# Kernel optimization log

Hardware: AMD Instinct MI355X
Metric: run time of the kernel (lower is better)

## Reference

```python
import jax, jax.numpy as jnp
import numpy as np

BS, TLEN, NNODE, DIM = 32, 6, 4, 1500
HID = 128; D2 = 2 * HID
LSTMH, LSTMO, KCONV = 64, 128, 3
CONV_OUT = 191
DECAY = 0.7
WIN, STRIDES = (2, 2), (1, 2)
FEAT_IN = LSTMO * CONV_OUT  # 24448


def _bn(x, p, axis):
    # eval-mode BatchNorm: p = [gamma, beta, running_mean, running_var] stacked [4, C]
    sh = [1] * x.ndim; sh[axis] = -1
    g, b, m, v = (p[i].reshape(sh) for i in range(4))
    return (x - m) * (g * jax.lax.rsqrt(v + 1e-5)) + b


def _conv1d(x, w, pad):  # x [B,C,L], w [O,I,K]
    return jax.lax.conv_general_dilated(x, w, (1,), [(pad, pad)],
                                        dimension_numbers=('NCH', 'OIH', 'NCH'))


def _maxpool2(x):  # MaxPool1d(kernel=2, stride=2, padding=1) with -inf padding
    x = jnp.pad(x, ((0, 0), (0, 0), (1, 1)), constant_values=-jnp.inf)
    return jax.lax.reduce_window(x, -jnp.inf, jax.lax.max, (1, 1, 2), (1, 1, 2), 'VALID')


def _mpnn_block(x, w, s, gw, gb, bnA, tw, tb, bnM):
    # x: [bs, tlen, ns, d]; Conv_GraphST windowing + dot-graph + masked adj + 1-hop MPNN + mean pool
    bs, tlen, ns, d = x.shape
    nw = (tlen - w) // s + 1
    con = jnp.stack([x[:, j * s:j * s + w] for j in range(nw)], axis=1)  # [bs,nw,w,ns,d]
    Xc = con.reshape(bs * nw, w * ns, d)  # node index = t*ns + sensor (time-major)
    f = Xc @ gw + gb
    N = w * ns
    eye = jnp.eye(N, dtype=x.dtype)
    Adj = jnp.einsum('bnd,bmd->bnm', f, f)
    Adj = jax.nn.softmax(jax.nn.leaky_relu(Adj - eye * 1e8), axis=-1) + eye
    t = jnp.arange(N) // ns
    mask = DECAY ** jnp.abs(t[:, None] - t[None, :]).astype(x.dtype)  # Mask_Matrix decay
    Adj = Adj * mask
    Xb = _bn(Xc, bnA, -1)  # BN over feature channel (transpose-BN-transpose in torch)
    h = jnp.einsum('bnm,bmd->bnd', Adj, Xb) @ tw + tb
    h = jax.nn.leaky_relu(_bn(h, bnM, -1))
    return h.reshape(bs, nw, w, ns, -1).mean(axis=2)  # mean pool over window-time


def _pos_encoding(tlen, d):
    pos = jnp.arange(tlen, dtype=jnp.float32)[:, None]
    div = jnp.exp(jnp.arange(0, d, 2, dtype=jnp.float32) * (-np.log(100.0) / d))
    pe = jnp.zeros((tlen, d), jnp.float32)
    return pe.at[:, 0::2].set(jnp.sin(pos * div)).at[:, 1::2].set(jnp.cos(pos * div))


def reference(X, conv1_w, bn1, conv2_w, bn2, conv3_w, bn3,
              map2_w, map2_b, bn_map2,
              g1_w, g1_b, bnA1, th1_w, th1_b, bnM1,
              g2_w, g2_b, bnA2, th2_w, th2_b, bnM2,
              fc1_w, fc1_b, fc2_w, fc2_b, fc3_w, fc3_b, fc4_w, fc4_b):
    X = X.reshape(BS, TLEN, NNODE, -1)
    B = BS * TLEN * NNODE
    a = jnp.transpose(X.reshape(B, -1, 1), (0, 2, 1))  # [B,1,L]
    a = _maxpool2(jax.nn.relu(_bn(_conv1d(a, conv1_w, KCONV // 2), bn1, 1)))
    a = _maxpool2(jax.nn.relu(_bn(_conv1d(a, conv2_w, 2), bn2, 1)))
    a = _maxpool2(jax.nn.relu(_bn(_conv1d(a, conv3_w, 3), bn3, 1)))  # [B,LSTMO,CONV_OUT]
    a = a.reshape(B, -1)
    a = _bn(a @ map2_w + map2_b, bn_map2, -1)
    a = a.reshape(BS, TLEN, NNODE, D2)
    a = a + _pos_encoding(TLEN, D2)[None, :, None, :]  # PE over time, per (batch, node)
    out1 = _mpnn_block(a, WIN[0], STRIDES[0], g1_w, g1_b, bnA1, th1_w, th1_b, bnM1)  # [32,5,4,128]
    out2 = _mpnn_block(a, WIN[1], STRIDES[1], g2_w, g2_b, bnA2, th2_w, th2_b, bnM2)  # [32,3,4,128]
    feats = jnp.concatenate([out1.reshape(BS, -1), out2.reshape(BS, -1)], axis=-1)  # [32,4096]
    h = jax.nn.relu(feats @ fc1_w + fc1_b)
    h = jax.nn.relu(h @ fc2_w + fc2_b)
    h = jax.nn.relu(h @ fc3_w + fc3_b)
    return h @ fc4_w + fc4_b


def setup_inputs():
    key = jax.random.key(0)
    ks = iter(jax.random.split(key, 80))
    def rn(shape, scale=1.0):
        return scale * jax.random.normal(next(ks), shape, jnp.float32)
    def bn(c):
        return jnp.stack([1.0 + 0.1 * rn((c,)), 0.1 * rn((c,)), 0.1 * rn((c,)),
                          1.0 + 0.5 * jax.random.uniform(next(ks), (c,), jnp.float32)])
    def lin(i, o):
        return rn((i, o), 1.0 / np.sqrt(i))
    return {
        'X': rn((BS, TLEN, NNODE, DIM)),
        'conv1_w': rn((LSTMH, 1, KCONV), 0.3),
        'bn1': bn(LSTMH),
        'conv2_w': rn((2 * LSTMH, LSTMH, KCONV), 1.0 / np.sqrt(LSTMH * KCONV)),
        'bn2': bn(2 * LSTMH),
        'conv3_w': rn((LSTMO, 2 * LSTMH, KCONV), 1.0 / np.sqrt(2 * LSTMH * KCONV)),
        'bn3': bn(LSTMO),
        'map2_w': lin(FEAT_IN, D2), 'map2_b': rn((D2,), 0.01), 'bn_map2': bn(D2),
        'g1_w': lin(D2, D2), 'g1_b': rn((D2,), 0.01), 'bnA1': bn(D2),
        'th1_w': lin(D2, HID), 'th1_b': rn((HID,), 0.01), 'bnM1': bn(HID),
        'g2_w': lin(D2, D2), 'g2_b': rn((D2,), 0.01), 'bnA2': bn(D2),
        'th2_w': lin(D2, HID), 'th2_b': rn((HID,), 0.01), 'bnM2': bn(HID),
        'fc1_w': lin(4096, D2), 'fc1_b': rn((D2,), 0.01),
        'fc2_w': lin(D2, D2), 'fc2_b': rn((D2,), 0.01),
        'fc3_w': lin(D2, HID), 'fc3_b': rn((HID,), 0.01),
        'fc4_w': lin(HID, 5), 'fc4_b': rn((5,), 0.01),
    }
```

## Files before the change

### kernel.cpp

```cpp
#include <hip/hip_runtime.h>
#include <hip/hip_bf16.h>

#define L1X   1500
#define L1P   751
#define C1    64
#define L2P   377
#define C2    128
#define L3P   191
#define C3    128
#define FEATK 24448
#define D2    256
#define HIDN  128

#define SK      32
#define KCHUNK  764
#define NIT     191

typedef __attribute__((ext_vector_type(8))) short bf16x8;
typedef __attribute__((ext_vector_type(4))) float f32x4;

__device__ __forceinline__ short f2bf(float x) {
    union { float f; unsigned u; } v; v.f = x;
    unsigned r = (v.u + 0x7FFFu + ((v.u >> 16) & 1u)) >> 16;
    return (short)r;
}
__device__ __forceinline__ float bf2f(short s) {
    union { float f; unsigned u; } v; v.u = ((unsigned)(unsigned short)s) << 16;
    return v.f;
}

template<int IC, int KB>
__global__ __launch_bounds__(256)
void k_wprep(const float* __restrict__ w, short* __restrict__ WtHi,
             short* __restrict__ WtLo)
{
    int idx = blockIdx.x * 256 + threadIdx.x;
    if (idx >= 3 * KB * 4 * 128 * 8) return;
    int i    = idx & 7;
    int rest = idx >> 3;
    int c    = rest & 127; rest >>= 7;
    int sub  = rest & 3;   rest >>= 2;
    int kb   = rest % KB;
    int tap  = rest / KB;
    int ic   = kb * 32 + sub * 8 + i;
    float x  = w[(c * IC + ic) * 3 + tap];
    short h  = f2bf(x);
    WtHi[idx] = h;
    WtLo[idx] = f2bf(x - bf2f(h));
}

template<int IC, int KB, int CONVLEN, int POOLLEN>
__device__ __forceinline__
void conv_mfma_core(const short* __restrict__ WtHi, const short* __restrict__ WtLo,
                    const short* lhi, const short* llo,
                    const float* sc, const float* bc,
                    float* __restrict__ outp, int P0)
{
    const int lane = threadIdx.x & 63;
    const int wave = threadIdx.x >> 6;
    const int l15  = lane & 15;
    const int sub  = lane >> 4;

    f32x4 acc[2][8];
    #pragma unroll
    for (int mf = 0; mf < 2; ++mf)
        #pragma unroll
        for (int nf = 0; nf < 8; ++nf)
            acc[mf][nf] = (f32x4){0.f, 0.f, 0.f, 0.f};

    #pragma unroll
    for (int tap = 0; tap < 3; ++tap) {
        #pragma unroll
        for (int kb = 0; kb < KB; ++kb) {
            bf16x8 ah[2], al[2];
            #pragma unroll
            for (int mf = 0; mf < 2; ++mf) {
                int r = wave * 32 + mf * 16 + l15 + tap;
                int chunk = (kb * 4 + sub) ^ (r & 7);
                int off = r * IC + chunk * 8;
                ah[mf] = *(const bf16x8*)(lhi + off);
                al[mf] = *(const bf16x8*)(llo + off);
            }
            const short* wbh = WtHi + (size_t)(((tap * KB + kb) * 4 + sub) * 128) * 8;
            const short* wbl = WtLo + (size_t)(((tap * KB + kb) * 4 + sub) * 128) * 8;
            #pragma unroll
            for (int nf = 0; nf < 8; ++nf) {
                bf16x8 bh = *(const bf16x8*)(wbh + (nf * 16 + l15) * 8);
                bf16x8 bl = *(const bf16x8*)(wbl + (nf * 16 + l15) * 8);
                #pragma unroll
                for (int mf = 0; mf < 2; ++mf) {
                    acc[mf][nf] = __builtin_amdgcn_mfma_f32_16x16x32_bf16(ah[mf], bh, acc[mf][nf], 0, 0, 0);
                    acc[mf][nf] = __builtin_amdgcn_mfma_f32_16x16x32_bf16(ah[mf], bl, acc[mf][nf], 0, 0, 0);
                    acc[mf][nf] = __builtin_amdgcn_mfma_f32_16x16x32_bf16(al[mf], bh, acc[mf][nf], 0, 0, 0);
                }
            }
        }
    }

    #pragma unroll
    for (int mf = 0; mf < 2; ++mf) {
        int mbase = wave * 32 + mf * 16 + sub * 4;
        #pragma unroll
        for (int nf = 0; nf < 8; ++nf) {
            int c = nf * 16 + l15;
            float s = sc[c], bb = bc[c];
            float v[4];
            #pragma unroll
            for (int rg = 0; rg < 4; ++rg) {
                int p = P0 + mbase + rg;
                float x = fmaxf(acc[mf][nf][rg] * s + bb, 0.f);
                v[rg] = (p >= 0 && p < CONVLEN) ? x : 0.f;
            }
            int i0 = (P0 + mbase + 1) >> 1;
            float u0 = fmaxf(v[0], v[1]);
            float u1 = fmaxf(v[2], v[3]);
            if (i0 < POOLLEN)     outp[(size_t)i0 * 128 + c] = u0;
            if (i0 + 1 < POOLLEN) outp[(size_t)(i0 + 1) * 128 + c] = u1;
        }
    }
}

__global__ __launch_bounds__(256)
void k_conv2_mfma(const float* __restrict__ X, const float* __restrict__ w1,
                  const float* __restrict__ bn1,
                  const short* __restrict__ Wt2hi, const short* __restrict__ Wt2lo,
                  const float* __restrict__ bn2, float* __restrict__ pool2t,
                  int b_off)
{
    const int blk = blockIdx.x;
    const int bl  = blk / 6, t = blk % 6;
    const int b   = b_off + bl;
    const int P0  = 128 * t - 1;
    const int T0  = 128 * t - 3;
    const int X0  = 256 * t - 8;

    __shared__ __align__(16) float xw[264];
    __shared__ __align__(16) short t1h[130 * 64];
    __shared__ __align__(16) short t1l[130 * 64];
    __shared__ float sb1s[64], sb1b[64], sc2[128], bc2[128];

    const int tid = threadIdx.x;
    for (int g = tid; g < 262; g += 256) {
        int xi = X0 + g;
        xw[g] = (xi >= 0 && xi < L1X) ? X[(size_t)b * L1X + xi] : 0.f;
    }
    if (tid < 64) {
        float s = bn1[tid] * rsqrtf(bn1[192 + tid] + 1e-5f);
        sb1s[tid] = s;
        sb1b[tid] = bn1[64 + tid] - bn1[128 + tid] * s;
    }
    if (tid < 128) {
        float s = bn2[tid] * rsqrtf(bn2[384 + tid] + 1e-5f);
        sc2[tid] = s;
        bc2[tid] = bn2[128 + tid] - bn2[256 + tid] * s;
    }
    __syncthreads();

    for (int idx = tid; idx < 130 * 64; idx += 256) {
        int r = idx >> 6, c = idx & 63;
        int tt = T0 + r;
        float val = 0.f;
        if (tt >= 0 && tt <= 750) {
            float wk0 = w1[c * 3], wk1 = w1[c * 3 + 1], wk2 = w1[c * 3 + 2];
            float s = sb1s[c], bias = sb1b[c];
            float v0 = 0.f, v1 = 0.f;
            int li = 2 * r;
            if (tt >= 1)
                v0 = fmaxf((wk0 * xw[li] + wk1 * xw[li + 1] + wk2 * xw[li + 2]) * s + bias, 0.f);
            if (tt <= 749)
                v1 = fmaxf((wk0 * xw[li + 1] + wk1 * xw[li + 2] + wk2 * xw[li + 3]) * s + bias, 0.f);
            val = fmaxf(v0, v1);
        }
        short h = f2bf(val);
        int chunk = (c >> 3) ^ (r & 7);
        int off = r * 64 + chunk * 8 + (c & 7);
        t1h[off] = h;
        t1l[off] = f2bf(val - bf2f(h));
    }
    __syncthreads();

    conv_mfma_core<64, 2, 753, 377>(Wt2hi, Wt2lo, t1h, t1l, sc2, bc2,
                                    pool2t + (size_t)bl * L2P * 128, P0);
}

__global__ __launch_bounds__(256)
void k_conv3_mfma(const float* __restrict__ pool2t,
                  const short* __restrict__ Wt3hi, const short* __restrict__ Wt3lo,
                  const float* __restrict__ bn3, float* __restrict__ pool3t,
                  int b_off)
{
    const int blk = blockIdx.x;
    const int bl  = blk / 3, t = blk % 3;
    const int b   = b_off + bl;
    const int P0  = 128 * t - 1;
    const int I0  = 128 * t - 4;

    __shared__ __align__(16) short t2h[130 * 128];
    __shared__ __align__(16) short t2l[130 * 128];
    __shared__ float sc3[128], bc3[128];

    const int tid = threadIdx.x;
    if (tid < 128) {
        float s = bn3[tid] * rsqrtf(bn3[384 + tid] + 1e-5f);
        sc3[tid] = s;
        bc3[tid] = bn3[128 + tid] - bn3[256 + tid] * s;
    }

    const float* src = pool2t + (size_t)bl * L2P * 128;
    for (int idx = tid; idx < 130 * 32; idx += 256) {
        int r = idx >> 5, q = idx & 31;
        int pr = I0 + r;
        float4 v = make_float4(0.f, 0.f, 0.f, 0.f);
        if (pr >= 0 && pr < L2P) v = *(const float4*)(src + (size_t)pr * 128 + q * 4);
        int chunk = (q >> 1) ^ (r & 7);
        int off = r * 128 + chunk * 8 + (q & 1) * 4;
        *(short4*)(t2h + off) = make_short4(f2bf(v.x), f2bf(v.y), f2bf(v.z), f2bf(v.w));
        short l0 = f2bf(v.x - bf2f(f2bf(v.x)));
        short l1 = f2bf(v.y - bf2f(f2bf(v.y)));
        short l2 = f2bf(v.z - bf2f(f2bf(v.z)));
        short l3 = f2bf(v.w - bf2f(f2bf(v.w)));
        *(short4*)(t2l + off) = make_short4(l0, l1, l2, l3);
    }
    __syncthreads();

    conv_mfma_core<128, 4, 381, 191>(Wt3hi, Wt3lo, t2h, t2l, sc3, bc3,
                                     pool3t + (size_t)b * L3P * 128, P0);
}

__global__ __launch_bounds__(256)
void k_map2_gemm(const float* __restrict__ A, const float* __restrict__ W,
                 float* __restrict__ part)
{
    const int bid = blockIdx.x;
    const int kt  = bid / 24;
    const int rem = bid % 24;
    const int mt  = rem >> 1;
    const int nt  = rem & 1;

    __shared__ __align__(16) float At[2][4][68];
    __shared__ __align__(16) float Bt[2][4][128];

    const int tid = threadIdx.x;
    const int m0  = (tid & 15) * 4;
    const int n0  = (tid >> 4) * 8;

    const int arow = tid >> 2;
    const int akk  = tid & 3;
    const int bk   = tid >> 6;
    const int bc   = (tid & 63) * 2;

    const float* Aptr = A + (size_t)(mt * 64 + arow) * FEATK + kt * KCHUNK + akk;

    #define BROW(it) (W + (size_t)((((kt*KCHUNK + (it)*4 + bk) & 127) * 191 + \
                                    ((kt*KCHUNK + (it)*4 + bk) >> 7))) * D2 + nt*128 + bc)

    float acc[4][8];
    #pragma unroll
    for (int i = 0; i < 4; ++i)
        #pragma unroll
        for (int j = 0; j < 8; ++j) acc[i][j] = 0.f;

    float  a_reg = Aptr[0];
    float2 b_reg = *(const float2*)(BROW(0));
    At[0][akk][arow] = a_reg;
    *(float2*)&Bt[0][bk][bc] = b_reg;

    int cur = 0;
    for (int it = 0; it < NIT; ++it) {
        __syncthreads();
        if (it + 1 < NIT) {
            a_reg = Aptr[(it + 1) * 4];
            b_reg = *(const float2*)(BROW(it + 1));
        }
        #pragma unroll
        for (int k = 0; k < 4; ++k) {
            float4 a0 = *(const float4*)&At[cur][k][m0];
            float4 b0 = *(const float4*)&Bt[cur][k][n0];
            float4 b1 = *(const float4*)&Bt[cur][k][n0 + 4];
            float av[4] = {a0.x, a0.y, a0.z, a0.w};
            float bv[8] = {b0.x, b0.y, b0.z, b0.w, b1.x, b1.y, b1.z, b1.w};
            #pragma unroll
            for (int i = 0; i < 4; ++i)
                #pragma unroll
                for (int j = 0; j < 8; ++j)
                    acc[i][j] += av[i] * bv[j];
        }
        if (it + 1 < NIT) {
            At[cur ^ 1][akk][arow] = a_reg;
            *(float2*)&Bt[cur ^ 1][bk][bc] = b_reg;
        }
        cur ^= 1;
    }
    #undef BROW

    float* P = part + ((size_t)kt * 768) * D2;
    #pragma unroll
    for (int i = 0; i < 4; ++i) {
        int grow = mt * 64 + m0 + i;
        float* dst = P + (size_t)grow * D2 + nt * 128 + n0;
        *(float4*)(dst)     = make_float4(acc[i][0], acc[i][1], acc[i][2], acc[i][3]);
        *(float4*)(dst + 4) = make_float4(acc[i][4], acc[i][5], acc[i][6], acc[i][7]);
    }
}

__global__ __launch_bounds__(256)
void k_map2fin(const float* __restrict__ part, const float* __restrict__ mb,
               const float* __restrict__ bn, float* __restrict__ out)
{
    const int row = blockIdx.x;
    const int n   = threadIdx.x;
    float acc = 0.f;
    #pragma unroll
    for (int kt = 0; kt < SK; ++kt)
        acc += part[((size_t)kt * 768 + row) * D2 + n];

    float s    = bn[n] * rsqrtf(bn[768 + n] + 1e-5f);
    float beta = bn[256 + n];
    float mu   = bn[512 + n];
    float bias = mb[n];
    int   jj   = n >> 1;
    float freq = expf((float)(2 * jj) * (-4.605170185988092f / 256.f));
    int   t    = (row >> 2) % 6;
    float ang  = (float)t * freq;
    float pe   = (n & 1) ? cosf(ang) : sinf(ang);
    out[(size_t)row * D2 + n] = (acc + bias - mu) * s + beta + pe;
}

__global__ __launch_bounds__(256)
void k_mpnn(const float* __restrict__ a_pe, const float* __restrict__ gw,
            const float* __restrict__ gb, const float* __restrict__ bnA,
            const float* __restrict__ tw, const float* __restrict__ tb_,
            const float* __restrict__ bnM, float* __restrict__ feats,
            int nw, int stride, int base)
{
    const int g  = blockIdx.x;
    const int b  = g / nw, wi = g % nw;
    const int tid = threadIdx.x;

    __shared__ float Xc[8][256];
    __shared__ float Xb[8][256];
    __shared__ float Fs[8][256];
    __shared__ float Adj[8][8];
    __shared__ float hsm[8][128];

    for (int e = tid; e < 2048; e += 256) {
        int nn = e >> 8, d = e & 255;
        int tt = nn >> 2, sn = nn & 3;
        float v = a_pe[(((size_t)(b * 6) + (wi * stride + tt)) * 4 + sn) * D2 + d];
        Xc[nn][d] = v;
        float s = bnA[d] * rsqrtf(bnA[768 + d] + 1e-5f);
        Xb[nn][d] = (v - bnA[512 + d]) * s + bnA[256 + d];
    }
    __syncthreads();

    {
        const int d = tid;
        #pragma unroll
        for (int nn = 0; nn < 8; ++nn) {
            float acc = gb[d];
            for (int k = 0; k < 256; ++k) acc += Xc[nn][k] * gw[(size_t)k * D2 + d];
            Fs[nn][d] = acc;
        }
    }
    __syncthreads();

    if (tid < 64) {
        int nn = tid >> 3, m = tid & 7;
        float s = 0.f;
        for (int d = 0; d < 256; ++d) s += Fs[nn][d] * Fs[m][d];
        if (nn == m) s -= 1e8f;
        s = (s > 0.f) ? s : 0.01f * s;
        Adj[nn][m] = s;
    }
    __syncthreads();

    if (tid < 8) {
        int nn = tid;
        float mx = -1e30f;
        for (int m = 0; m < 8; ++m) mx = fmaxf(mx, Adj[nn][m]);
        float ex[8]; float sum = 0.f;
        for (int m = 0; m < 8; ++m) { ex[m] = expf(Adj[nn][m] - mx); sum += ex[m]; }
        float inv = 1.f / sum;
        for (int m = 0; m < 8; ++m) {
            float v = ex[m] * inv + ((nn == m) ? 1.f : 0.f);
            v *= ((nn >> 2) == (m >> 2)) ? 1.f : 0.7f;
            Adj[nn][m] = v;
        }
    }
    __syncthreads();

    {
        const int d = tid;
        float hm[8];
        #pragma unroll
        for (int nn = 0; nn < 8; ++nn) {
            float a = 0.f;
            #pragma unroll
            for (int m = 0; m < 8; ++m) a += Adj[nn][m] * Xb[m][d];
            hm[nn] = a;
        }
        #pragma unroll
        for (int nn = 0; nn < 8; ++nn) Fs[nn][d] = hm[nn];
    }
    __syncthreads();

    {
        const int o = tid & 127, half = tid >> 7;
        float ms  = bnM[o] * rsqrtf(bnM[384 + o] + 1e-5f);
        float mbe = bnM[128 + o], mmu = bnM[256 + o];
        #pragma unroll
        for (int q = 0; q < 4; ++q) {
            int nn = half + 2 * q;
            float acc = tb_[o];
            for (int d = 0; d < 256; ++d) acc += Fs[nn][d] * tw[(size_t)d * HIDN + o];
            float y = (acc - mmu) * ms + mbe;
            hsm[nn][o] = (y > 0.f) ? y : 0.01f * y;
        }
    }
    __syncthreads();

    for (int e = tid; e < 512; e += 256) {
        int sn = e >> 7, o = e & 127;
        feats[(size_t)b * 4096 + base + (wi * 4 + sn) * HIDN + o] =
            0.5f * (hsm[sn][o] + hsm[4 + sn][o]);
    }
}

__global__ __launch_bounds__(256)
void k_fc1(const float* __restrict__ feats, const float* __restrict__ w1f,
           float* __restrict__ partfc)
{
    const int kc = blockIdx.x >> 3;
    const int nc = blockIdx.x & 7;
    const int tid = threadIdx.x;

    __shared__ float fst[32 * 257];

    for (int idx = tid; idx < 32 * 256; idx += 256) {
        int r = idx >> 8, k = idx & 255;
        fst[r * 257 + k] = feats[(size_t)r * 4096 + kc * 256 + k];
    }
    __syncthreads();

    const int c  = tid & 31;
    const int rg = tid >> 5;
    const float* wp = w1f + (size_t)(kc * 256) * 256 + nc * 32 + c;

    float acc[4] = {0.f, 0.f, 0.f, 0.f};
    for (int k = 0; k < 256; ++k) {
        float wv = wp[(size_t)k * 256];
        #pragma unroll
        for (int j = 0; j < 4; ++j)
            acc[j] += fst[(rg * 4 + j) * 257 + k] * wv;
    }
    #pragma unroll
    for (int j = 0; j < 4; ++j)
        partfc[((size_t)kc * 32 + rg * 4 + j) * 256 + nc * 32 + c] = acc[j];
}

__global__ __launch_bounds__(256)
void k_fc_rest(const float* __restrict__ partfc,
               const float* __restrict__ b1f,
               const float* __restrict__ w2f, const float* __restrict__ b2f,
               const float* __restrict__ w3f, const float* __restrict__ b3f,
               const float* __restrict__ w4f, const float* __restrict__ b4f,
               float* __restrict__ out)
{
    const int b = blockIdx.x;
    const int n = threadIdx.x;
    __shared__ float h1[256], h2[256], h3[128];

    {
        float acc = b1f[n];
        #pragma unroll
        for (int kc = 0; kc < 16; ++kc)
            acc += partfc[((size_t)kc * 32 + b) * 256 + n];
        h1[n] = fmaxf(acc, 0.f);
    }
    __syncthreads();
    {
        float acc = b2f[n];
        for (int k = 0; k < 256; ++k) acc += h1[k] * w2f[(size_t)k * 256 + n];
        h2[n] = fmaxf(acc, 0.f);
    }
    __syncthreads();
    if (n < 128) {
        float acc = b3f[n];
        for (int k = 0; k < 256; ++k) acc += h2[k] * w3f[(size_t)k * 128 + n];
        h3[n] = fmaxf(acc, 0.f);
    }
    __syncthreads();
    if (n < 5) {
        float acc = b4f[n];
        for (int k = 0; k < 128; ++k) acc += h3[k] * w4f[(size_t)k * 5 + n];
        out[b * 5 + n] = acc;
    }
}

extern "C" void kernel_launch(void* const* d_in, const int* in_sizes, int n_in,
                              void* d_out, int out_size, void* d_ws, size_t ws_size,
                              hipStream_t stream)
{
    const float* X      = (const float*)d_in[0];
    const float* w1     = (const float*)d_in[1];
    const float* bn1    = (const float*)d_in[2];
    const float* w2     = (const float*)d_in[3];
    const float* bn2    = (const float*)d_in[4];
    const float* w3     = (const float*)d_in[5];
    const float* bn3    = (const float*)d_in[6];
    const float* map2w  = (const float*)d_in[7];
    const float* map2b  = (const float*)d_in[8];
    const float* bnm2   = (const float*)d_in[9];
    const float* g1w    = (const float*)d_in[10];
    const float* g1b    = (const float*)d_in[11];
    const float* bnA1   = (const float*)d_in[12];
    const float* th1w   = (const float*)d_in[13];
    const float* th1b   = (const float*)d_in[14];
    const float* bnM1   = (const float*)d_in[15];
    const float* g2w    = (const float*)d_in[16];
    const float* g2b    = (const float*)d_in[17];
    const float* bnA2   = (const float*)d_in[18];
    const float* th2w   = (const float*)d_in[19];
    const float* th2b   = (const float*)d_in[20];
    const float* bnM2   = (const float*)d_in[21];
    const float* fc1w   = (const float*)d_in[22];
    const float* fc1b   = (const float*)d_in[23];
    const float* fc2w   = (const float*)d_in[24];
    const float* fc2b   = (const float*)d_in[25];
    const float* fc3w   = (const float*)d_in[26];
    const float* fc3b   = (const float*)d_in[27];
    const float* fc4w   = (const float*)d_in[28];
    const float* fc4b   = (const float*)d_in[29];
    float* out = (float*)d_out;

    float* ws = (float*)d_ws;
    const size_t N_P2C = (size_t)192 * L2P * 128;
    const size_t N_P3  = (size_t)768 * L3P * 128;
    float* pool2t = ws;
    float* pool3t = ws + N_P2C;
    float* a_pe   = pool3t + N_P3;
    float* feats  = a_pe + (size_t)768 * D2;
    short* Wt2hi  = (short*)(feats + (size_t)32 * 4096);
    short* Wt2lo  = Wt2hi + 24576;
    short* Wt3hi  = Wt2lo + 24576;
    short* Wt3lo  = Wt3hi + 49152;
    float* partfc = (float*)(Wt3lo + 49152);
    float* part   = ws;

    k_wprep<64, 2><<<96, 256, 0, stream>>>(w2, Wt2hi, Wt2lo);
    k_wprep<128, 4><<<192, 256, 0, stream>>>(w3, Wt3hi, Wt3lo);

    for (int boff = 0; boff < 768; boff += 192) {
        k_conv2_mfma<<<192 * 6, 256, 0, stream>>>(X, w1, bn1, Wt2hi, Wt2lo, bn2,
                                                  pool2t, boff);
        k_conv3_mfma<<<192 * 3, 256, 0, stream>>>(pool2t, Wt3hi, Wt3lo, bn3,
                                                  pool3t, boff);
    }
    k_map2_gemm<<<768, 256, 0, stream>>>(pool3t, map2w, part);
    k_map2fin<<<768, 256, 0, stream>>>(part, map2b, bnm2, a_pe);
    k_mpnn<<<160, 256, 0, stream>>>(a_pe, g1w, g1b, bnA1, th1w, th1b, bnM1,
                                    feats, 5, 1, 0);
    k_mpnn<<<96, 256, 0, stream>>>(a_pe, g2w, g2b, bnA2, th2w, th2b, bnM2,
                                   feats, 3, 2, 2560);
    k_fc1<<<128, 256, 0, stream>>>(feats, fc1w, partfc);
    k_fc_rest<<<32, 256, 0, stream>>>(partfc, fc1b, fc2w, fc2b, fc3w, fc3b,
                                      fc4w, fc4b, out);
}
```

Measured before the change: 717.9 us.

## Move map2 GEMM to split-bf16 MFMA with atomic split-K accumulation

```diff
diff --git a/kernel.cpp b/kernel.cpp
--- a/kernel.cpp
+++ b/kernel.cpp
@@ -11,10 +11,7 @@
 #define FEATK 24448
 #define D2    256
 #define HIDN  128
-
-#define SK      32
-#define KCHUNK  764
-#define NIT     191
+#define KSTEPS 764
 
 typedef __attribute__((ext_vector_type(8))) short bf16x8;
 typedef __attribute__((ext_vector_type(4))) float f32x4;
@@ -49,12 +46,43 @@
     WtLo[idx] = f2bf(x - bf2f(h));
 }
 
-template<int IC, int KB, int CONVLEN, int POOLLEN>
+__global__ __launch_bounds__(256)
+void k_wmprep(const float* __restrict__ W, short* __restrict__ Wmhi,
+              short* __restrict__ Wmlo)
+{
+    const int ks  = blockIdx.x >> 2;
+    const int sub = blockIdx.x & 3;
+    const int n   = threadIdx.x;
+    const int kbase = ks * 32 + sub * 8;
+    bf16x8 vh, vl;
+    #pragma unroll
+    for (int i = 0; i < 8; ++i) {
+        int k = kbase + i;
+        int c = k & 127, ip = k >> 7;
+        float x = W[(size_t)(c * 191 + ip) * D2 + n];
+        short h = f2bf(x);
+        vh[i] = h;
+        vl[i] = f2bf(x - bf2f(h));
+    }
+    size_t off = ((size_t)(ks * 4 + sub) * 256 + n) * 8;
+    *(bf16x8*)(Wmhi + off) = vh;
+    *(bf16x8*)(Wmlo + off) = vl;
+}
+
+__global__ __launch_bounds__(256)
+void k_zero(float* __restrict__ p, int n)
+{
+    int i = blockIdx.x * 256 + threadIdx.x;
+    if (i < n) p[i] = 0.f;
+}
+
+template<int IC, int KB, int CONVLEN, int POOLLEN, bool HL>
 __device__ __forceinline__
 void conv_mfma_core(const short* __restrict__ WtHi, const short* __restrict__ WtLo,
                     const short* lhi, const short* llo,
                     const float* sc, const float* bc,
-                    float* __restrict__ outp, int P0)
+                    float* __restrict__ outp, short* __restrict__ ohi,
+                    short* __restrict__ olo, int P0)
 {
     const int lane = threadIdx.x & 63;
     const int wave = threadIdx.x >> 6;
@@ -114,8 +142,21 @@
             int i0 = (P0 + mbase + 1) >> 1;
             float u0 = fmaxf(v[0], v[1]);
             float u1 = fmaxf(v[2], v[3]);
-            if (i0 < POOLLEN)     outp[(size_t)i0 * 128 + c] = u0;
-            if (i0 + 1 < POOLLEN) outp[(size_t)(i0 + 1) * 128 + c] = u1;
+            if constexpr (HL) {
+                if (i0 < POOLLEN) {
+                    short h = f2bf(u0);
+                    ohi[(size_t)i0 * 128 + c] = h;
+                    olo[(size_t)i0 * 128 + c] = f2bf(u0 - bf2f(h));
+                }
+                if (i0 + 1 < POOLLEN) {
+                    short h = f2bf(u1);
+                    ohi[(size_t)(i0 + 1) * 128 + c] = h;
+                    olo[(size_t)(i0 + 1) * 128 + c] = f2bf(u1 - bf2f(h));
+                }
+            } else {
+                if (i0 < POOLLEN)     outp[(size_t)i0 * 128 + c] = u0;
+                if (i0 + 1 < POOLLEN) outp[(size_t)(i0 + 1) * 128 + c] = u1;
+            }
         }
     }
 }
@@ -179,15 +220,16 @@
     }
     __syncthreads();
 
-    conv_mfma_core<64, 2, 753, 377>(Wt2hi, Wt2lo, t1h, t1l, sc2, bc2,
-                                    pool2t + (size_t)bl * L2P * 128, P0);
+    conv_mfma_core<64, 2, 753, 377, false>(Wt2hi, Wt2lo, t1h, t1l, sc2, bc2,
+                                           pool2t + (size_t)bl * L2P * 128,
+                                           nullptr, nullptr, P0);
 }
 
 __global__ __launch_bounds__(256)
 void k_conv3_mfma(const float* __restrict__ pool2t,
                   const short* __restrict__ Wt3hi, const short* __restrict__ Wt3lo,
-                  const float* __restrict__ bn3, float* __restrict__ pool3t,
-                  int b_off)
+                  const float* __restrict__ bn3, short* __restrict__ p3hi,
+                  short* __restrict__ p3lo, int b_off)
 {
     const int blk = blockIdx.x;
     const int bl  = blk / 3, t = blk % 3;
@@ -223,96 +265,96 @@
     }
     __syncthreads();
 
-    conv_mfma_core<128, 4, 381, 191>(Wt3hi, Wt3lo, t2h, t2l, sc3, bc3,
-                                     pool3t + (size_t)b * L3P * 128, P0);
-}
-
-__global__ __launch_bounds__(256)
-void k_map2_gemm(const float* __restrict__ A, const float* __restrict__ W,
-                 float* __restrict__ part)
-{
-    const int bid = blockIdx.x;
-    const int kt  = bid / 24;
-    const int rem = bid % 24;
-    const int mt  = rem >> 1;
-    const int nt  = rem & 1;
-
-    __shared__ __align__(16) float At[2][4][68];
-    __shared__ __align__(16) float Bt[2][4][128];
-
-    const int tid = threadIdx.x;
-    const int m0  = (tid & 15) * 4;
-    const int n0  = (tid >> 4) * 8;
-
-    const int arow = tid >> 2;
-    const int akk  = tid & 3;
-    const int bk   = tid >> 6;
-    const int bc   = (tid & 63) * 2;
-
-    const float* Aptr = A + (size_t)(mt * 64 + arow) * FEATK + kt * KCHUNK + akk;
-
-    #define BROW(it) (W + (size_t)((((kt*KCHUNK + (it)*4 + bk) & 127) * 191 + \
-                                    ((kt*KCHUNK + (it)*4 + bk) >> 7))) * D2 + nt*128 + bc)
-
-    float acc[4][8];
+    conv_mfma_core<128, 4, 381, 191, true>(Wt3hi, Wt3lo, t2h, t2l, sc3, bc3,
+                                           nullptr,
+                                           p3hi + (size_t)b * FEATK,
+                                           p3lo + (size_t)b * FEATK, P0);
+}
+
+__global__ __launch_bounds__(256)
+void k_map2_mfma(const short* __restrict__ Ahi, const short* __restrict__ Alo,
+                 const short* __restrict__ Wmhi, const short* __restrict__ Wmlo,
+                 float* __restrict__ accum)
+{
+    const int kt   = blockIdx.x & 31;
+    const int mt   = blockIdx.x >> 5;
+    const int tid  = threadIdx.x;
+    const int lane = tid & 63, wave = tid >> 6;
+    const int l15  = lane & 15, sub = lane >> 4;
+    const int wm   = wave >> 1, wn = wave & 1;
+    const int m0   = mt * 64;
+
+    const int s0 = kt * 24;
+    const int s1 = (s0 + 24 < KSTEPS) ? s0 + 24 : KSTEPS;
+
+    __shared__ __align__(16) short Ah[2][64 * 40];
+    __shared__ __align__(16) short Al[2][64 * 40];
+
+    const int r  = tid >> 2;
+    const int kb = tid & 3;
+    const size_t abase = (size_t)(m0 + r) * FEATK + kb * 8;
+    const int    lbase = r * 40 + kb * 8;
+
+    f32x4 acc[2][8];
     #pragma unroll
-    for (int i = 0; i < 4; ++i)
-        #pragma unroll
-        for (int j = 0; j < 8; ++j) acc[i][j] = 0.f;
-
-    float  a_reg = Aptr[0];
-    float2 b_reg = *(const float2*)(BROW(0));
-    At[0][akk][arow] = a_reg;
-    *(float2*)&Bt[0][bk][bc] = b_reg;
+    for (int mf = 0; mf < 2; ++mf)
+        #pragma unroll
+        for (int nf = 0; nf < 8; ++nf)
+            acc[mf][nf] = (f32x4){0.f, 0.f, 0.f, 0.f};
+
+    *(bf16x8*)&Ah[0][lbase] = *(const bf16x8*)(Ahi + abase + (size_t)s0 * 32);
+    *(bf16x8*)&Al[0][lbase] = *(const bf16x8*)(Alo + abase + (size_t)s0 * 32);
 
     int cur = 0;
-    for (int it = 0; it < NIT; ++it) {
+    for (int s = s0; s < s1; ++s) {
         __syncthreads();
-        if (it + 1 < NIT) {
-            a_reg = Aptr[(it + 1) * 4];
-            b_reg = *(const float2*)(BROW(it + 1));
-        }
-        #pragma unroll
-        for (int k = 0; k < 4; ++k) {
-            float4 a0 = *(const float4*)&At[cur][k][m0];
-            float4 b0 = *(const float4*)&Bt[cur][k][n0];
-            float4 b1 = *(const float4*)&Bt[cur][k][n0 + 4];
-            float av[4] = {a0.x, a0.y, a0.z, a0.w};
-            float bv[8] = {b0.x, b0.y, b0.z, b0.w, b1.x, b1.y, b1.z, b1.w};
+        if (s + 1 < s1) {
+            *(bf16x8*)&Ah[cur ^ 1][lbase] = *(const bf16x8*)(Ahi + abase + (size_t)(s + 1) * 32);
+            *(bf16x8*)&Al[cur ^ 1][lbase] = *(const bf16x8*)(Alo + abase + (size_t)(s + 1) * 32);
+        }
+        bf16x8 ah[2], al[2];
+        #pragma unroll
+        for (int mf = 0; mf < 2; ++mf) {
+            int off = (wm * 32 + mf * 16 + l15) * 40 + sub * 8;
+            ah[mf] = *(const bf16x8*)&Ah[cur][off];
+            al[mf] = *(const bf16x8*)&Al[cur][off];
+        }
+        const short* wb = Wmhi + ((size_t)(s * 4 + sub) * 256 + wn * 128) * 8;
+        const short* wl = Wmlo + ((size_t)(s * 4 + sub) * 256 + wn * 128) * 8;
+        #pragma unroll
+        for (int nf = 0; nf < 8; ++nf) {
+            bf16x8 bh = *(const bf16x8*)(wb + (nf * 16 + l15) * 8);
+            bf16x8 bl = *(const bf16x8*)(wl + (nf * 16 + l15) * 8);
             #pragma unroll
-            for (int i = 0; i < 4; ++i)
-                #pragma unroll
-                for (int j = 0; j < 8; ++j)
-                    acc[i][j] += av[i] * bv[j];
-        }
-        if (it + 1 < NIT) {
-            At[cur ^ 1][akk][arow] = a_reg;
-            *(float2*)&Bt[cur ^ 1][bk][bc] = b_reg;
+            for (int mf = 0; mf < 2; ++mf) {
+                acc[mf][nf] = __builtin_amdgcn_mfma_f32_16x16x32_bf16(ah[mf], bh, acc[mf][nf], 0, 0, 0);
+                acc[mf][nf] = __builtin_amdgcn_mfma_f32_16x16x32_bf16(ah[mf], bl, acc[mf][nf], 0, 0, 0);
+                acc[mf][nf] = __builtin_amdgcn_mfma_f32_16x16x32_bf16(al[mf], bh, acc[mf][nf], 0, 0, 0);
+            }
         }
         cur ^= 1;
     }
-    #undef BROW
-
-    float* P = part + ((size_t)kt * 768) * D2;
+
     #pragma unroll
-    for (int i = 0; i < 4; ++i) {
-        int grow = mt * 64 + m0 + i;
-        float* dst = P + (size_t)grow * D2 + nt * 128 + n0;
-        *(float4*)(dst)     = make_float4(acc[i][0], acc[i][1], acc[i][2], acc[i][3]);
-        *(float4*)(dst + 4) = make_float4(acc[i][4], acc[i][5], acc[i][6], acc[i][7]);
-    }
-}
-
-__global__ __launch_bounds__(256)
-void k_map2fin(const float* __restrict__ part, const float* __restrict__ mb,
+    for (int mf = 0; mf < 2; ++mf) {
+        int mrow = m0 + wm * 32 + mf * 16 + sub * 4;
+        #pragma unroll
+        for (int nf = 0; nf < 8; ++nf) {
+            int n = wn * 128 + nf * 16 + l15;
+            #pragma unroll
+            for (int rg = 0; rg < 4; ++rg)
+                atomicAdd(&accum[(size_t)(mrow + rg) * D2 + n], acc[mf][nf][rg]);
+        }
+    }
+}
+
+__global__ __launch_bounds__(256)
+void k_map2fin(const float* __restrict__ accum, const float* __restrict__ mb,
                const float* __restrict__ bn, float* __restrict__ out)
 {
     const int row = blockIdx.x;
     const int n   = threadIdx.x;
-    float acc = 0.f;
-    #pragma unroll
-    for (int kt = 0; kt < SK; ++kt)
-        acc += part[((size_t)kt * 768 + row) * D2 + n];
+    float acc = accum[(size_t)row * D2 + n];
 
     float s    = bn[n] * rsqrtf(bn[768 + n] + 1e-5f);
     float beta = bn[256 + n];
@@ -534,30 +576,33 @@
     float* out = (float*)d_out;
 
     float* ws = (float*)d_ws;
-    const size_t N_P2C = (size_t)192 * L2P * 128;
-    const size_t N_P3  = (size_t)768 * L3P * 128;
     float* pool2t = ws;
-    float* pool3t = ws + N_P2C;
-    float* a_pe   = pool3t + N_P3;
-    float* feats  = a_pe + (size_t)768 * D2;
-    short* Wt2hi  = (short*)(feats + (size_t)32 * 4096);
+    short* p3hi   = (short*)(ws + 4632576);
+    short* p3lo   = p3hi + 18776064;
+    float* a_pe   = (float*)(p3lo + 18776064);
+    float* feats  = a_pe + 196608;
+    short* Wt2hi  = (short*)(feats + 131072);
     short* Wt2lo  = Wt2hi + 24576;
     short* Wt3hi  = Wt2lo + 24576;
     short* Wt3lo  = Wt3hi + 49152;
     float* partfc = (float*)(Wt3lo + 49152);
-    float* part   = ws;
+    short* Wmhi   = (short*)(partfc + 131072);
+    short* Wmlo   = Wmhi + 6258688;
+    float* accum  = ws;
 
     k_wprep<64, 2><<<96, 256, 0, stream>>>(w2, Wt2hi, Wt2lo);
     k_wprep<128, 4><<<192, 256, 0, stream>>>(w3, Wt3hi, Wt3lo);
-
-    for (int boff = 0; boff < 768; boff += 192) {
-        k_conv2_mfma<<<192 * 6, 256, 0, stream>>>(X, w1, bn1, Wt2hi, Wt2lo, bn2,
-                                                  pool2t, boff);
-        k_conv3_mfma<<<192 * 3, 256, 0, stream>>>(pool2t, Wt3hi, Wt3lo, bn3,
-                                                  pool3t, boff);
-    }
-    k_map2_gemm<<<768, 256, 0, stream>>>(pool3t, map2w, part);
-    k_map2fin<<<768, 256, 0, stream>>>(part, map2b, bnm2, a_pe);
+    k_wmprep<<<KSTEPS * 4, 256, 0, stream>>>(map2w, Wmhi, Wmlo);
+
+    for (int boff = 0; boff < 768; boff += 96) {
+        k_conv2_mfma<<<96 * 6, 256, 0, stream>>>(X, w1, bn1, Wt2hi, Wt2lo, bn2,
+                                                 pool2t, boff);
+        k_conv3_mfma<<<96 * 3, 256, 0, stream>>>(pool2t, Wt3hi, Wt3lo, bn3,
+                                                 p3hi, p3lo, boff);
+    }
+    k_zero<<<768, 256, 0, stream>>>(accum, 196608);
+    k_map2_mfma<<<384, 256, 0, stream>>>(p3hi, p3lo, Wmhi, Wmlo, accum);
+    k_map2fin<<<768, 256, 0, stream>>>(accum, map2b, bnm2, a_pe);
     k_mpnn<<<160, 256, 0, stream>>>(a_pe, g1w, g1b, bnA1, th1w, th1b, bnM1,
                                     feats, 5, 1, 0);
     k_mpnn<<<96, 256, 0, stream>>>(a_pe, g2w, g2b, bnA2, th2w, th2b, bnM2,
```

After: 742.8 us. 1.03x slower.
